# Kernel tuning notes

Measured on AMD Instinct MI355X. Metric: run time of the kernel, lower is better.

## Reference

```python
import jax, jax.numpy as jnp
import numpy as np

D_MODEL = 768
N_HEAD = 12
D_FF = 2048
KEEP_RATIO = 0.6
EPS = 1e-6


def rmsnorm(x, g):
    var = jnp.mean(x * x, axis=-1, keepdims=True)
    return x * jax.lax.rsqrt(var + EPS) * g


def setup_inputs() -> dict:
    key = jax.random.key(0)
    ks = jax.random.split(key, 16)
    B, S, D, F = 2, 2048, D_MODEL, D_FF
    s = 0.02
    inp = {
        "hidden": jax.random.normal(ks[0], (B, S, D), jnp.float32),
        "attn_mask": jnp.tril(jnp.ones((S, S), dtype=bool)),
        "temperature": 1,
        "wq": jax.random.normal(ks[1], (D, D), jnp.float32) * s,
        "wk": jax.random.normal(ks[2], (D, D), jnp.float32) * s,
        "wv": jax.random.normal(ks[3], (D, D), jnp.float32) * s,
        "wo": jax.random.normal(ks[4], (D, D), jnp.float32) * s,
        "w1": jax.random.normal(ks[5], (D, F), jnp.float32) * s,
        "w3": jax.random.normal(ks[6], (D, F), jnp.float32) * s,
        "w2": jax.random.normal(ks[7], (F, D), jnp.float32) * s,
        "g1": jnp.ones((D,), jnp.float32),
        "g2": jnp.ones((D,), jnp.float32),
        "w_mod": jax.random.normal(ks[8], (D,), jnp.float32) * s,
        "b_mod": jnp.zeros((), jnp.float32),
        "w_tok": jax.random.normal(ks[9], (D,), jnp.float32) * s,
        "b_tok": jnp.zeros((), jnp.float32),
        "w_gate": jax.random.normal(ks[10], (D, D), jnp.float32) * s,
        "b_gate": jnp.zeros((D,), jnp.float32),
    }
    return inp


def reference(hidden, attn_mask, temperature, wq, wk, wv, wo, w1, w3, w2,
              g1, g2, w_mod, b_mod, w_tok, b_tok, w_gate, b_gate):
    B, S, D = hidden.shape
    H = N_HEAD
    Dh = D // H

    # depth router: sigmoid(linear / temperature)
    depth_logits = jnp.einsum("bsd,d->bs", hidden, w_mod) + b_mod
    depth_probs = jax.nn.sigmoid(depth_logits / temperature)
    active = (depth_probs > 0.5).astype(hidden.dtype)[..., None]  # [B,S,1]

    normed = rmsnorm(hidden, g1)

    # token router: sigmoid scores, hard top-k keep mask at base keep ratio
    token_scores = jax.nn.sigmoid(jnp.einsum("bsd,d->bs", normed, w_tok) + b_tok)
    k = max(1, int(S * KEEP_RATIO))
    kth = jax.lax.top_k(token_scores, k)[0][:, -1:]  # [B,1]
    token_mask = (token_scores >= kth).astype(hidden.dtype)  # [B,S]

    # multi-head attention over normed
    q = jnp.einsum("bsd,de->bse", normed, wq).reshape(B, S, H, Dh)
    kk = jnp.einsum("bsd,de->bse", normed, wk).reshape(B, S, H, Dh)
    v = jnp.einsum("bsd,de->bse", normed, wv).reshape(B, S, H, Dh)
    logits = jnp.einsum("bqhd,bkhd->bhqk", q, kk) / jnp.sqrt(jnp.float32(Dh))
    logits = jnp.where(attn_mask[None, None, :, :], logits, jnp.float32(-1e9))
    probs = jax.nn.softmax(logits, axis=-1)
    ctx = jnp.einsum("bhqk,bkhd->bqhd", probs, v).reshape(B, S, D)
    attn_out = jnp.einsum("bsd,de->bse", ctx, wo)

    attn_out = attn_out * token_mask[..., None]
    hidden = hidden + attn_out * active  # dropout = identity (eval)

    # ACM gate: x * sigmoid(Wx + b)
    n2 = rmsnorm(hidden, g2)
    gated = n2 * jax.nn.sigmoid(jnp.einsum("bsd,de->bse", n2, w_gate) + b_gate)

    # SwiGLU MLP
    mlp = jnp.einsum("bsf,fd->bsd",
                     jax.nn.silu(jnp.einsum("bsd,df->bsf", gated, w1))
                     * jnp.einsum("bsd,df->bsf", gated, w3), w2)
    hidden = hidden + mlp * active
    return hidden, depth_probs, token_mask
```

## Files before the change

kernel.cpp:

```cpp
#include <hip/hip_runtime.h>


typedef float f32x4 __attribute__((ext_vector_type(4)));
typedef __bf16 bf16x8 __attribute__((ext_vector_type(8)));
typedef __bf16 bf16x4 __attribute__((ext_vector_type(4)));
typedef unsigned int u32;

#define DEV static __device__ __forceinline__

constexpr int SEQ = 2048, DIM = 768, NH = 12;
constexpr int KKEEP = 1228;
constexpr float SCALE2 = 0.125f * 1.4426950408889634f;

DEV f32x4 mfma16(bf16x8 a, bf16x8 b, f32x4 c) {
  return __builtin_amdgcn_mfma_f32_16x16x32_bf16(a, b, c, 0, 0, 0);
}
DEV float sigm(float x) { return 1.0f / (1.0f + __expf(-x)); }
DEV bf16x8 ld8(const __bf16* p) { return *reinterpret_cast<const bf16x8*>(p); }
DEV void st8(__bf16* p, bf16x8 v) { *reinterpret_cast<bf16x8*>(p) = v; }
DEV int swzo(int row, int u) { return row * 64 + ((u ^ (row & 7)) << 3); }

template <int NZ>
struct PtrPack { const float* s[NZ]; };

template <int NZ>
__global__ void k_transpose_castz(PtrPack<NZ> pp, __bf16* __restrict__ dst0,
                                  int K, int N, size_t dstride) {
  const float* __restrict__ src = pp.s[blockIdx.z];
  __bf16* __restrict__ dst = dst0 + (size_t)blockIdx.z * dstride;
  __shared__ float tile[32][33];
  const int tx = threadIdx.x, ty = threadIdx.y;
  const int n0 = blockIdx.x * 32, k0 = blockIdx.y * 32;
  for (int i = 0; i < 4; ++i)
    tile[ty + 8 * i][tx] = src[(size_t)(k0 + ty + 8 * i) * N + n0 + tx];
  __syncthreads();
  for (int i = 0; i < 4; ++i)
    dst[(size_t)(n0 + ty + 8 * i) * K + k0 + tx] = (__bf16)tile[tx][ty + 8 * i];
}

__global__ __launch_bounds__(256) void k_router(
    const float* __restrict__ hid, const float* __restrict__ g1,
    const float* __restrict__ wmod, const float* __restrict__ bmod,
    const float* __restrict__ wtok, const float* __restrict__ btok,
    const int* __restrict__ temp, __bf16* __restrict__ normed,
    float* __restrict__ depth_out, float* __restrict__ actF,
    float* __restrict__ tokL) {
  const int t = blockIdx.x, tid = threadIdx.x;
  const float* x = hid + (size_t)t * DIM;
  float xs[3], gs[3], ss = 0.f, dm = 0.f, dt = 0.f;
  for (int j = 0; j < 3; ++j) {
    const int i = tid + 256 * j;
    const float xv = x[i], g = g1[i];
    xs[j] = xv; gs[j] = g;
    ss += xv * xv;
    dm += xv * wmod[i];
    dt += xv * g * wtok[i];
  }
  for (int m = 32; m >= 1; m >>= 1) {
    ss += __shfl_xor(ss, m);
    dm += __shfl_xor(dm, m);
    dt += __shfl_xor(dt, m);
  }
  __shared__ float red[4][3];
  if ((tid & 63) == 0) { red[tid >> 6][0] = ss; red[tid >> 6][1] = dm; red[tid >> 6][2] = dt; }
  __syncthreads();
  ss = red[0][0] + red[1][0] + red[2][0] + red[3][0];
  dm = red[0][1] + red[1][1] + red[2][1] + red[3][1];
  dt = red[0][2] + red[1][2] + red[2][2] + red[3][2];
  const float rms = rsqrtf(ss / 768.0f + 1e-6f);
  if (tid == 0) {
    const int iv = temp[0];
    const float T = (iv > -100000 && iv < 100000) ? (float)iv : __int_as_float(iv);
    const float z = (dm + bmod[0]) / T;
    depth_out[t] = sigm(z);
    actF[t] = z > 0.0f ? 1.0f : 0.0f;
    tokL[t] = rms * dt + btok[0];
  }
  for (int j = 0; j < 3; ++j) {
    const int i = tid + 256 * j;
    normed[(size_t)t * DIM + i] = (__bf16)(xs[j] * rms * gs[j]);
  }
}

__global__ __launch_bounds__(256) void k_count(
    const float* __restrict__ tokL, float* __restrict__ kth_out) {
  const int b = blockIdx.y, tid = threadIdx.x;
  __shared__ float vals[2048];
  const float* L = tokL + (size_t)b * 2048;
#pragma unroll
  for (int j = 0; j < 8; ++j) vals[tid + 256 * j] = L[tid + 256 * j];
  __syncthreads();
  const int cand = blockIdx.x * 128 + (tid >> 1);
  const int half = tid & 1;
  const float e = vals[cand];
  int gt = 0, ge = 0;
  const float4* v4 = reinterpret_cast<const float4*>(vals) + half * 256;
#pragma unroll 8
  for (int j = 0; j < 256; ++j) {
    const float4 q = v4[j];
    gt += (q.x > e) + (q.y > e) + (q.z > e) + (q.w > e);
    ge += (q.x >= e) + (q.y >= e) + (q.z >= e) + (q.w >= e);
  }
  gt += __shfl_xor(gt, 1);
  ge += __shfl_xor(ge, 1);
  if (half == 0 && gt < KKEEP && KKEEP <= ge) kth_out[b] = e;
}

__global__ __launch_bounds__(256) void k_mask(
    const float* __restrict__ tokL, const float* __restrict__ kth,
    const float* __restrict__ actF, float* __restrict__ mask_out,
    float* __restrict__ maskact) {
  const int i = blockIdx.x * 256 + threadIdx.x;
  const int b = i >> 11;
  const float m = (tokL[i] >= kth[b]) ? 1.f : 0.f;
  mask_out[i] = m;
  maskact[i] = m * actF[i];
}

__global__ __launch_bounds__(256) void k_rmsnorm2(
    const float* __restrict__ h2, const float* __restrict__ g2,
    __bf16* __restrict__ n2) {
  const int t = blockIdx.x, tid = threadIdx.x;
  const float* x = h2 + (size_t)t * DIM;
  float xs[3], ss = 0.f;
  for (int j = 0; j < 3; ++j) { const float v = x[tid + 256 * j]; xs[j] = v; ss += v * v; }
  for (int m = 32; m >= 1; m >>= 1) ss += __shfl_xor(ss, m);
  __shared__ float red[4];
  if ((tid & 63) == 0) red[tid >> 6] = ss;
  __syncthreads();
  ss = red[0] + red[1] + red[2] + red[3];
  const float rms = rsqrtf(ss / 768.0f + 1e-6f);
  for (int j = 0; j < 3; ++j) {
    const int i = tid + 256 * j;
    n2[(size_t)t * DIM + i] = (__bf16)(xs[j] * rms * g2[i]);
  }
}

template <int EPI, int MI, int NI>
__global__ __launch_bounds__(256) void k_gemm(
    const __bf16* __restrict__ A, const __bf16* __restrict__ BT,
    int N, int K, size_t bt_stride, size_t out_stride,
    __bf16* __restrict__ outB, float* __restrict__ outF,
    const float* __restrict__ epF, const __bf16* __restrict__ epB,
    const float* __restrict__ rowsc, const float* __restrict__ bias) {
  constexpr int BM = MI * 32, BN = NI * 32;
  __shared__ __align__(16) __bf16 As[BM * 64];
  __shared__ __align__(16) __bf16 Bs[BN * 64];
  const int tid = threadIdx.x;
  const int lane = tid & 63, w = tid >> 6;
  const int wr = w >> 1, wc = w & 1;
  const int f = lane & 15, e = lane >> 4;
  const int m0 = blockIdx.y * BM, n0 = blockIdx.x * BN;
  const __bf16* Bz = BT + (size_t)blockIdx.z * bt_stride;

  const int rowA = (MI == 4) ? (tid >> 1) : (tid >> 2);
  const int uA0  = (MI == 4) ? ((tid & 1) * 4) : ((tid & 3) * 2);
  const int rowB = (NI == 4) ? (tid >> 1) : (tid >> 2);
  const int uB0  = (NI == 4) ? ((tid & 1) * 4) : ((tid & 3) * 2);
  const __bf16* ApR = A + (size_t)(m0 + rowA) * K;
  const __bf16* BpR = Bz + (size_t)(n0 + rowB) * K;

  bf16x8 ya[MI], yb[NI];
  auto LOADY = [&](int k0) {
#pragma unroll
    for (int j = 0; j < MI; ++j) ya[j] = ld8(ApR + k0 + (uA0 + j) * 8);
#pragma unroll
    for (int j = 0; j < NI; ++j) yb[j] = ld8(BpR + k0 + (uB0 + j) * 8);
  };
  auto STORE = [&]() {
#pragma unroll
    for (int j = 0; j < MI; ++j) st8(&As[swzo(rowA, uA0 + j)], ya[j]);
#pragma unroll
    for (int j = 0; j < NI; ++j) st8(&Bs[swzo(rowB, uB0 + j)], yb[j]);
  };

  f32x4 acc[MI][NI] = {};
  LOADY(0);
  for (int k0 = 0; k0 < K; k0 += 64) {
    __syncthreads();
    STORE();
    if (k0 + 64 < K) LOADY(k0 + 64);
    __syncthreads();
    bf16x8 afl[MI], afh[MI], bfl[NI], bfh[NI];
#pragma unroll
    for (int mi = 0; mi < MI; ++mi) {
      const int row = wr * (MI * 16) + mi * 16 + f;
      afl[mi] = ld8(&As[swzo(row, e)]);
      afh[mi] = ld8(&As[swzo(row, e + 4)]);
    }
#pragma unroll
    for (int ni = 0; ni < NI; ++ni) {
      const int row = wc * (NI * 16) + ni * 16 + f;
      bfl[ni] = ld8(&Bs[swzo(row, e)]);
      bfh[ni] = ld8(&Bs[swzo(row, e + 4)]);
    }
#pragma unroll
    for (int mi = 0; mi < MI; ++mi)
#pragma unroll
      for (int ni = 0; ni < NI; ++ni) {
        acc[mi][ni] = mfma16(afl[mi], bfl[ni], acc[mi][ni]);
        acc[mi][ni] = mfma16(afh[mi], bfh[ni], acc[mi][ni]);
      }
  }
  const size_t oz = (size_t)blockIdx.z * out_stride;
  if constexpr (EPI == 5) {
    __bf16* vt = (__bf16*)outF;
    const bool isv = (blockIdx.z == 2);
    const float qs = (blockIdx.z == 0) ? SCALE2 : 1.0f;
#pragma unroll
    for (int mi = 0; mi < MI; ++mi)
#pragma unroll
      for (int ni = 0; ni < NI; ++ni) {
        const int row0 = m0 + wr * (MI * 16) + mi * 16 + e * 4;
        const int col = n0 + wc * (NI * 16) + ni * 16 + f;
        if (!isv) {
#pragma unroll
          for (int r2 = 0; r2 < 4; ++r2)
            outB[oz + (size_t)(row0 + r2) * N + col] =
                (__bf16)(acc[mi][ni][r2] * qs);
        } else {
          bf16x4 pk;
#pragma unroll
          for (int r2 = 0; r2 < 4; ++r2) pk[r2] = (__bf16)acc[mi][ni][r2];
          *reinterpret_cast<bf16x4*>(&vt[(size_t)col * 4096 + row0]) = pk;
        }
      }
  } else {
#pragma unroll
    for (int mi = 0; mi < MI; ++mi)
#pragma unroll
      for (int ni = 0; ni < NI; ++ni)
#pragma unroll
        for (int r2 = 0; r2 < 4; ++r2) {
          const int row = m0 + wr * (MI * 16) + mi * 16 + e * 4 + r2;
          const int col = n0 + wc * (NI * 16) + ni * 16 + f;
          const size_t idx = (size_t)row * N + col;
          const float c = acc[mi][ni][r2];
          if constexpr (EPI == 0) {
            outB[oz + idx] = (__bf16)c;
          } else if constexpr (EPI == 1) {
            outF[idx] = epF[idx] + c * rowsc[row];
          } else if constexpr (EPI == 2) {
            outB[idx] = (__bf16)((float)epB[idx] * sigm(c + bias[col]));
          }
        }
  }
}

__global__ __launch_bounds__(256) void k_gemm13(
    const __bf16* __restrict__ A, const __bf16* __restrict__ B1T,
    const __bf16* __restrict__ B3T, __bf16* __restrict__ outT) {
  __shared__ __align__(16) __bf16 As[64 * 64];
  __shared__ __align__(16) __bf16 B1s[128 * 64];
  __shared__ __align__(16) __bf16 B3s[128 * 64];
  const int tid = threadIdx.x;
  const int lane = tid & 63, w = tid >> 6;
  const int wr = w >> 1, wc = w & 1;
  const int f = lane & 15, e = lane >> 4;
  const int m0 = blockIdx.y * 64, n0 = blockIdx.x * 128;
  const int rowA = tid >> 2, uA0 = (tid & 3) * 2;
  const int rowB = tid >> 1, uB0 = (tid & 1) * 4;
  const __bf16* ApR = A + (size_t)(m0 + rowA) * 768;
  const __bf16* B1R = B1T + (size_t)(n0 + rowB) * 768;
  const __bf16* B3R = B3T + (size_t)(n0 + rowB) * 768;

  bf16x8 ya[2], yb1[4], yb3[4];
  auto LOADY = [&](int k0) {
#pragma unroll
    for (int j = 0; j < 2; ++j) ya[j] = ld8(ApR + k0 + (uA0 + j) * 8);
#pragma unroll
    for (int j = 0; j < 4; ++j) yb1[j] = ld8(B1R + k0 + (uB0 + j) * 8);
#pragma unroll
    for (int j = 0; j < 4; ++j) yb3[j] = ld8(B3R + k0 + (uB0 + j) * 8);
  };
  auto STORE = [&]() {
#pragma unroll
    for (int j = 0; j < 2; ++j) st8(&As[swzo(rowA, uA0 + j)], ya[j]);
#pragma unroll
    for (int j = 0; j < 4; ++j) st8(&B1s[swzo(rowB, uB0 + j)], yb1[j]);
#pragma unroll
    for (int j = 0; j < 4; ++j) st8(&B3s[swzo(rowB, uB0 + j)], yb3[j]);
  };

  f32x4 acc1[2][4] = {}, acc3[2][4] = {};
  LOADY(0);
  for (int k0 = 0; k0 < 768; k0 += 64) {
    __syncthreads();
    STORE();
    if (k0 + 64 < 768) LOADY(k0 + 64);
    __syncthreads();
    bf16x8 afl[2], afh[2], bl[4], bh[4];
#pragma unroll
    for (int mi = 0; mi < 2; ++mi) {
      const int row = wr * 32 + mi * 16 + f;
      afl[mi] = ld8(&As[swzo(row, e)]);
      afh[mi] = ld8(&As[swzo(row, e + 4)]);
    }
#pragma unroll
    for (int ni = 0; ni < 4; ++ni) {
      const int row = wc * 64 + ni * 16 + f;
      bl[ni] = ld8(&B1s[swzo(row, e)]);
      bh[ni] = ld8(&B1s[swzo(row, e + 4)]);
    }
#pragma unroll
    for (int mi = 0; mi < 2; ++mi)
#pragma unroll
      for (int ni = 0; ni < 4; ++ni) {
        acc1[mi][ni] = mfma16(afl[mi], bl[ni], acc1[mi][ni]);
        acc1[mi][ni] = mfma16(afh[mi], bh[ni], acc1[mi][ni]);
      }
#pragma unroll
    for (int ni = 0; ni < 4; ++ni) {
      const int row = wc * 64 + ni * 16 + f;
      bl[ni] = ld8(&B3s[swzo(row, e)]);
      bh[ni] = ld8(&B3s[swzo(row, e + 4)]);
    }
#pragma unroll
    for (int mi = 0; mi < 2; ++mi)
#pragma unroll
      for (int ni = 0; ni < 4; ++ni) {
        acc3[mi][ni] = mfma16(afl[mi], bl[ni], acc3[mi][ni]);
        acc3[mi][ni] = mfma16(afh[mi], bh[ni], acc3[mi][ni]);
      }
  }
#pragma unroll
  for (int mi = 0; mi < 2; ++mi)
#pragma unroll
    for (int ni = 0; ni < 4; ++ni)
#pragma unroll
      for (int r2 = 0; r2 < 4; ++r2) {
        const int row = m0 + wr * 32 + mi * 16 + e * 4 + r2;
        const int col = n0 + wc * 64 + ni * 16 + f;
        const float u = acc1[mi][ni][r2];
        outT[(size_t)row * 2048 + col] = (__bf16)(u * sigm(u) * acc3[mi][ni][r2]);
      }
}

__global__ __launch_bounds__(256) void k_attn(
    const __bf16* __restrict__ qb, const __bf16* __restrict__ kb,
    const __bf16* __restrict__ vT, __bf16* __restrict__ Opart,
    float* __restrict__ ml) {
  __shared__ __bf16 Ks[64 * 64];
  __shared__ __bf16 Vt[64 * 64];
  __shared__ __bf16 Pl[4][16][72];
  const int tid = threadIdx.x, lane = tid & 63, w = tid >> 6;
  const int f = lane & 15, e = lane >> 4;
  const int idx = 79 - (int)blockIdx.x;
  int g4, rel;
  if (idx < 8)       { g4 = 0; rel = idx; }
  else if (idx < 24) { g4 = 1; rel = idx - 8; }
  else if (idx < 48) { g4 = 2; rel = idx - 24; }
  else               { g4 = 3; rel = idx - 48; }
  const int qt = (g4 << 3) + rel / (g4 + 1);
  const int c  = rel % (g4 + 1);
  const int bh = blockIdx.y;
  const int b = bh / NH, h = bh % NH;
  const int slot = bh * 80 + idx;
  const int q0 = qt * 64;
  const int kt0 = c * 8;
  const int ntile = min(8, qt + 1 - kt0);
  const size_t base = (size_t)b * SEQ * DIM + (size_t)h * 64;

  const int qrow = q0 + w * 16 + f;
  const bf16x8 aq0 = ld8(qb + base + (size_t)qrow * DIM + e * 8);
  const bf16x8 aq1 = ld8(qb + base + (size_t)qrow * DIM + 32 + e * 8);
  float lsum[4] = {0.f, 0.f, 0.f, 0.f};
  f32x4 cacc[4];
  for (int g = 0; g < 4; ++g) cacc[g] = f32x4{0.f, 0.f, 0.f, 0.f};

  const int r1 = tid >> 2, u0 = tid & 3;
  const __bf16* kp = kb + base + (size_t)r1 * DIM;
  const __bf16* vp = vT + (size_t)(h * 64 + r1) * 4096 + b * 2048;

  bf16x8 rk0 = ld8(kp + (size_t)(kt0 * 64) * DIM + u0 * 8);
  bf16x8 rk1 = ld8(kp + (size_t)(kt0 * 64) * DIM + (u0 + 4) * 8);
  bf16x8 rv0 = ld8(vp + kt0 * 64 + u0 * 8);
  bf16x8 rv1 = ld8(vp + kt0 * 64 + (u0 + 4) * 8);

  for (int tt = 0; tt < ntile; ++tt) {
    const int kt = kt0 + tt;
    __syncthreads();
    st8(&Ks[swzo(r1, u0)], rk0);  st8(&Ks[swzo(r1, u0 + 4)], rk1);
    st8(&Vt[swzo(r1, u0)], rv0);  st8(&Vt[swzo(r1, u0 + 4)], rv1);
    if (tt + 1 < ntile) {
      const size_t ko = (size_t)((kt + 1) * 64) * DIM;
      rk0 = ld8(kp + ko + u0 * 8);  rk1 = ld8(kp + ko + (u0 + 4) * 8);
      const int vo = (kt + 1) * 64;
      rv0 = ld8(vp + vo + u0 * 8);  rv1 = ld8(vp + vo + (u0 + 4) * 8);
    }
    __syncthreads();

    f32x4 sacc[4];
#pragma unroll
    for (int g = 0; g < 4; ++g) {
      const int row = g * 16 + f;
      f32x4 z = f32x4{0.f, 0.f, 0.f, 0.f};
      z = mfma16(aq0, ld8(&Ks[swzo(row, e)]), z);
      z = mfma16(aq1, ld8(&Ks[swzo(row, e + 4)]), z);
      sacc[g] = z;
    }
    const bool need_mask = (kt == qt);
    const int qg = q0 + w * 16 + e * 4;
    float p[4][4];
#pragma unroll
    for (int g = 0; g < 4; ++g) {
      const int kg = kt * 64 + g * 16 + f;
#pragma unroll
      for (int r = 0; r < 4; ++r) {
        const float pv = (need_mask && (kg > qg + r))
                             ? 0.f
                             : exp2f(sacc[g][r]);
        p[g][r] = pv;
        lsum[r] += pv;
      }
    }
#pragma unroll
    for (int g = 0; g < 4; ++g)
#pragma unroll
      for (int r = 0; r < 4; ++r) Pl[w][e * 4 + r][g * 16 + f] = (__bf16)p[g][r];
    const bf16x8 ap0 = ld8(&Pl[w][f][e * 8]);
    const bf16x8 ap1 = ld8(&Pl[w][f][32 + e * 8]);
#pragma unroll
    for (int g = 0; g < 4; ++g) {
      const int row = g * 16 + f;
      cacc[g] = mfma16(ap0, ld8(&Vt[swzo(row, e)]), cacc[g]);
      cacc[g] = mfma16(ap1, ld8(&Vt[swzo(row, e + 4)]), cacc[g]);
    }
  }
  for (int m = 1; m < 16; m <<= 1)
#pragma unroll
    for (int r = 0; r < 4; ++r) lsum[r] += __shfl_xor(lsum[r], m);
  if (f == 0) {
#pragma unroll
    for (int r = 0; r < 4; ++r)
      ml[(size_t)slot * 64 + w * 16 + e * 4 + r] = lsum[r];
  }
#pragma unroll
  for (int g = 0; g < 4; ++g)
#pragma unroll
    for (int r = 0; r < 4; ++r) {
      const int row = w * 16 + e * 4 + r;
      Opart[(size_t)slot * 4096 + row * 64 + g * 16 + f] = (__bf16)cacc[g][r];
    }
}

__global__ __launch_bounds__(256) void k_attn_combine(
    const __bf16* __restrict__ Opart, const float* __restrict__ ml,
    __bf16* __restrict__ ctxb) {
  const int qt = blockIdx.x, bh = blockIdx.y;
  const int b = bh / NH, h = bh % NH;
  const int g = qt >> 3;
  const int sb = bh * 80 + 4 * g * (g + 1) + (qt & 7) * (g + 1);
  const int nch = g + 1;
  const int row = threadIdx.x >> 2, dh0 = (threadIdx.x & 3) * 16;

  float ltot = 0.f;
  float acc[16];
#pragma unroll
  for (int j = 0; j < 16; ++j) acc[j] = 0.f;
  for (int cc = 0; cc < nch; ++cc) {
    ltot += ml[(size_t)(sb + cc) * 64 + row];
    const __bf16* op = Opart + (size_t)(sb + cc) * 4096 + row * 64 + dh0;
    const bf16x8 o0 = ld8(op), o1 = ld8(op + 8);
#pragma unroll
    for (int j = 0; j < 8; ++j) {
      acc[j] += (float)o0[j];
      acc[8 + j] += (float)o1[j];
    }
  }
  const float rl = 1.0f / ltot;
  bf16x8 w0, w1;
#pragma unroll
  for (int j = 0; j < 8; ++j) {
    w0[j] = (__bf16)(acc[j] * rl);
    w1[j] = (__bf16)(acc[8 + j] * rl);
  }
  const size_t base = (size_t)b * SEQ * DIM + (size_t)h * 64;
  __bf16* dst = ctxb + base + (size_t)(qt * 64 + row) * DIM + dh0;
  st8(dst, w0);
  st8(dst + 8, w1);
}

extern "C" void kernel_launch(void* const* d_in, const int* in_sizes, int n_in,
                              void* d_out, int out_size, void* d_ws, size_t ws_size,
                              hipStream_t stream) {
  const float* hid   = (const float*)d_in[0];
  const int*   temp  = (const int*)d_in[2];
  const float* wq    = (const float*)d_in[3];
  const float* wk    = (const float*)d_in[4];
  const float* wv    = (const float*)d_in[5];
  const float* wo    = (const float*)d_in[6];
  const float* w1    = (const float*)d_in[7];
  const float* w3    = (const float*)d_in[8];
  const float* w2    = (const float*)d_in[9];
  const float* g1    = (const float*)d_in[10];
  const float* g2    = (const float*)d_in[11];
  const float* wmod  = (const float*)d_in[12];
  const float* bmod  = (const float*)d_in[13];
  const float* wtok  = (const float*)d_in[14];
  const float* btok  = (const float*)d_in[15];
  const float* wgate = (const float*)d_in[16];
  const float* bgate = (const float*)d_in[17];

  char* ws = (char*)d_ws;
  __bf16* WT = (__bf16*)ws;
  const size_t oWQ = 0, oWK = 589824, oWV = 1179648, oWO = 1769472,
               oWG = 2359296, oW1 = 2949120, oW3 = 4521984, oW2 = 6094848;
  __bf16* qbuf   = (__bf16*)(ws + 15335424);
  __bf16* kbuf   = qbuf + 3145728;
  __bf16* vTbuf  = kbuf + 3145728;
  __bf16* normed = (__bf16*)(ws + 34209792);
  __bf16* ctxb   = normed + 3145728;
  __bf16* n2buf  = ctxb + 3145728;
  __bf16* tbuf   = normed;
  float*  h2     = (float*)(ws + 53084160);
  __bf16* gated  = (__bf16*)(ws + 65667072);
  __bf16* Opart  = (__bf16*)(ws + 53084160);
  float*  mlbuf  = (float*)(ws + 68812800);
  float*  tokL   = (float*)(ws + 71958528);
  float*  actF   = tokL + 4096;
  float*  maskact = actF + 4096;
  float*  kthbuf  = maskact + 4096;

  float* dout = (float*)d_out;
  float* out_hidden = dout;
  float* out_depth  = dout + 3145728;
  float* out_mask   = dout + 3145728 + 4096;

  const dim3 tb(32, 8);
  PtrPack<5> p5; p5.s[0]=wq; p5.s[1]=wk; p5.s[2]=wv; p5.s[3]=wo; p5.s[4]=wgate;
  k_transpose_castz<5><<<dim3(24, 24, 5), tb, 0, stream>>>(p5, WT + oWQ, 768, 768, 589824);
  PtrPack<2> p2; p2.s[0]=w1; p2.s[1]=w3;
  k_transpose_castz<2><<<dim3(64, 24, 2), tb, 0, stream>>>(p2, WT + oW1, 768, 2048, 1572864);
  PtrPack<1> p1; p1.s[0]=w2;
  k_transpose_castz<1><<<dim3(24, 64, 1), tb, 0, stream>>>(p1, WT + oW2, 2048, 768, 0);

  k_router<<<4096, 256, 0, stream>>>(hid, g1, wmod, bmod, wtok, btok, temp,
                                     normed, out_depth, actF, tokL);
  k_count<<<dim3(16, 2), 256, 0, stream>>>(tokL, kthbuf);
  k_mask<<<16, 256, 0, stream>>>(tokL, kthbuf, actF, out_mask, maskact);

  k_gemm<5, 4, 4><<<dim3(6, 32, 3), 256, 0, stream>>>(
      normed, WT + oWQ, 768, 768, 589824, 3145728,
      qbuf, (float*)vTbuf, nullptr, nullptr, nullptr, nullptr);

  k_attn<<<dim3(80, 24), 256, 0, stream>>>(qbuf, kbuf, vTbuf, Opart, mlbuf);
  k_attn_combine<<<dim3(32, 24), 256, 0, stream>>>(Opart, mlbuf, ctxb);

  k_gemm<1, 2, 2><<<dim3(12, 64, 1), 256, 0, stream>>>(
      ctxb, WT + oWO, 768, 768, 0, 0,
      nullptr, h2, hid, nullptr, maskact, nullptr);

  k_rmsnorm2<<<4096, 256, 0, stream>>>(h2, g2, n2buf);

  k_gemm<2, 2, 2><<<dim3(12, 64, 1), 256, 0, stream>>>(
      n2buf, WT + oWG, 768, 768, 0, 0,
      gated, nullptr, nullptr, n2buf, nullptr, bgate);

  k_gemm13<<<dim3(16, 64), 256, 0, stream>>>(gated, WT + oW1, WT + oW3, tbuf);

  k_gemm<1, 2, 2><<<dim3(12, 64, 1), 256, 0, stream>>>(
      tbuf, WT + oW2, 768, 2048, 0, 0,
      nullptr, out_hidden, h2, nullptr, actF, nullptr);

  (void)in_sizes; (void)n_in; (void)out_size; (void)ws_size;
}
```

Before: 199.9 us.

## Interleave W1/W3 columns and reuse generic GEMM with a SwiGLU epilogue

The w1 and w3 weights are transposed into one row-interleaved matrix, so a single generic GEMM with N=4096 computes both projections. A new epilogue pairs adjacent columns with a lane shuffle and writes silu(u)*v. This replaces the dedicated dual-B gemm13 kernel with the larger-tile 4x4 GEMM path. Separately, the attention loop splits the diagonal-masked tile from unmasked tiles so the mask compare is skipped off the diagonal. In exchange, half the lanes sit idle during the SwiGLU store.

```diff
diff --git a/kernel.cpp b/kernel.cpp
--- a/kernel.cpp
+++ b/kernel.cpp
@@ -23,19 +23,25 @@
 template <int NZ>
 struct PtrPack { const float* s[NZ]; };
 
-template <int NZ>
+template <int NZ, int ILV = 0>
 __global__ void k_transpose_castz(PtrPack<NZ> pp, __bf16* __restrict__ dst0,
                                   int K, int N, size_t dstride) {
   const float* __restrict__ src = pp.s[blockIdx.z];
-  __bf16* __restrict__ dst = dst0 + (size_t)blockIdx.z * dstride;
   __shared__ float tile[32][33];
   const int tx = threadIdx.x, ty = threadIdx.y;
   const int n0 = blockIdx.x * 32, k0 = blockIdx.y * 32;
   for (int i = 0; i < 4; ++i)
     tile[ty + 8 * i][tx] = src[(size_t)(k0 + ty + 8 * i) * N + n0 + tx];
   __syncthreads();
-  for (int i = 0; i < 4; ++i)
-    dst[(size_t)(n0 + ty + 8 * i) * K + k0 + tx] = (__bf16)tile[tx][ty + 8 * i];
+  if constexpr (ILV) {
+    for (int i = 0; i < 4; ++i)
+      dst0[((size_t)(n0 + ty + 8 * i) * 2 + blockIdx.z) * K + k0 + tx] =
+          (__bf16)tile[tx][ty + 8 * i];
+  } else {
+    __bf16* __restrict__ dst = dst0 + (size_t)blockIdx.z * dstride;
+    for (int i = 0; i < 4; ++i)
+      dst[(size_t)(n0 + ty + 8 * i) * K + k0 + tx] = (__bf16)tile[tx][ty + 8 * i];
+  }
 }
 
 __global__ __launch_bounds__(256) void k_router(
@@ -225,6 +231,22 @@
           *reinterpret_cast<bf16x4*>(&vt[(size_t)col * 4096 + row0]) = pk;
         }
       }
+  } else if constexpr (EPI == 6) {
+    const int NO = N >> 1;
+#pragma unroll
+    for (int mi = 0; mi < MI; ++mi)
+#pragma unroll
+      for (int ni = 0; ni < NI; ++ni)
+#pragma unroll
+        for (int r2 = 0; r2 < 4; ++r2) {
+          const float mine = acc[mi][ni][r2];
+          const float part = __shfl_xor(mine, 1);
+          if ((f & 1) == 0) {
+            const int row = m0 + wr * (MI * 16) + mi * 16 + e * 4 + r2;
+            const int j = (n0 + wc * (NI * 16) + ni * 16 + f) >> 1;
+            outB[(size_t)row * NO + j] = (__bf16)(mine * sigm(mine) * part);
+          }
+        }
   } else {
 #pragma unroll
     for (int mi = 0; mi < MI; ++mi)
@@ -245,95 +267,6 @@
           }
         }
   }
-}
-
-__global__ __launch_bounds__(256) void k_gemm13(
-    const __bf16* __restrict__ A, const __bf16* __restrict__ B1T,
-    const __bf16* __restrict__ B3T, __bf16* __restrict__ outT) {
-  __shared__ __align__(16) __bf16 As[64 * 64];
-  __shared__ __align__(16) __bf16 B1s[128 * 64];
-  __shared__ __align__(16) __bf16 B3s[128 * 64];
-  const int tid = threadIdx.x;
-  const int lane = tid & 63, w = tid >> 6;
-  const int wr = w >> 1, wc = w & 1;
-  const int f = lane & 15, e = lane >> 4;
-  const int m0 = blockIdx.y * 64, n0 = blockIdx.x * 128;
-  const int rowA = tid >> 2, uA0 = (tid & 3) * 2;
-  const int rowB = tid >> 1, uB0 = (tid & 1) * 4;
-  const __bf16* ApR = A + (size_t)(m0 + rowA) * 768;
-  const __bf16* B1R = B1T + (size_t)(n0 + rowB) * 768;
-  const __bf16* B3R = B3T + (size_t)(n0 + rowB) * 768;
-
-  bf16x8 ya[2], yb1[4], yb3[4];
-  auto LOADY = [&](int k0) {
-#pragma unroll
-    for (int j = 0; j < 2; ++j) ya[j] = ld8(ApR + k0 + (uA0 + j) * 8);
-#pragma unroll
-    for (int j = 0; j < 4; ++j) yb1[j] = ld8(B1R + k0 + (uB0 + j) * 8);
-#pragma unroll
-    for (int j = 0; j < 4; ++j) yb3[j] = ld8(B3R + k0 + (uB0 + j) * 8);
-  };
-  auto STORE = [&]() {
-#pragma unroll
-    for (int j = 0; j < 2; ++j) st8(&As[swzo(rowA, uA0 + j)], ya[j]);
-#pragma unroll
-    for (int j = 0; j < 4; ++j) st8(&B1s[swzo(rowB, uB0 + j)], yb1[j]);
-#pragma unroll
-    for (int j = 0; j < 4; ++j) st8(&B3s[swzo(rowB, uB0 + j)], yb3[j]);
-  };
-
-  f32x4 acc1[2][4] = {}, acc3[2][4] = {};
-  LOADY(0);
-  for (int k0 = 0; k0 < 768; k0 += 64) {
-    __syncthreads();
-    STORE();
-    if (k0 + 64 < 768) LOADY(k0 + 64);
-    __syncthreads();
-    bf16x8 afl[2], afh[2], bl[4], bh[4];
-#pragma unroll
-    for (int mi = 0; mi < 2; ++mi) {
-      const int row = wr * 32 + mi * 16 + f;
-      afl[mi] = ld8(&As[swzo(row, e)]);
-      afh[mi] = ld8(&As[swzo(row, e + 4)]);
-    }
-#pragma unroll
-    for (int ni = 0; ni < 4; ++ni) {
-      const int row = wc * 64 + ni * 16 + f;
-      bl[ni] = ld8(&B1s[swzo(row, e)]);
-      bh[ni] = ld8(&B1s[swzo(row, e + 4)]);
-    }
-#pragma unroll
-    for (int mi = 0; mi < 2; ++mi)
-#pragma unroll
-      for (int ni = 0; ni < 4; ++ni) {
-        acc1[mi][ni] = mfma16(afl[mi], bl[ni], acc1[mi][ni]);
-        acc1[mi][ni] = mfma16(afh[mi], bh[ni], acc1[mi][ni]);
-      }
-#pragma unroll
-    for (int ni = 0; ni < 4; ++ni) {
-      const int row = wc * 64 + ni * 16 + f;
-      bl[ni] = ld8(&B3s[swzo(row, e)]);
-      bh[ni] = ld8(&B3s[swzo(row, e + 4)]);
-    }
-#pragma unroll
-    for (int mi = 0; mi < 2; ++mi)
-#pragma unroll
-      for (int ni = 0; ni < 4; ++ni) {
-        acc3[mi][ni] = mfma16(afl[mi], bl[ni], acc3[mi][ni]);
-        acc3[mi][ni] = mfma16(afh[mi], bh[ni], acc3[mi][ni]);
-      }
-  }
-#pragma unroll
-  for (int mi = 0; mi < 2; ++mi)
-#pragma unroll
-    for (int ni = 0; ni < 4; ++ni)
-#pragma unroll
-      for (int r2 = 0; r2 < 4; ++r2) {
-        const int row = m0 + wr * 32 + mi * 16 + e * 4 + r2;
-        const int col = n0 + wc * 64 + ni * 16 + f;
-        const float u = acc1[mi][ni][r2];
-        outT[(size_t)row * 2048 + col] = (__bf16)(u * sigm(u) * acc3[mi][ni][r2]);
-      }
 }
 
 __global__ __launch_bounds__(256) void k_attn(
@@ -399,20 +332,28 @@
       z = mfma16(aq1, ld8(&Ks[swzo(row, e + 4)]), z);
       sacc[g] = z;
     }
-    const bool need_mask = (kt == qt);
-    const int qg = q0 + w * 16 + e * 4;
     float p[4][4];
-#pragma unroll
-    for (int g = 0; g < 4; ++g) {
-      const int kg = kt * 64 + g * 16 + f;
-#pragma unroll
-      for (int r = 0; r < 4; ++r) {
-        const float pv = (need_mask && (kg > qg + r))
-                             ? 0.f
-                             : exp2f(sacc[g][r]);
-        p[g][r] = pv;
-        lsum[r] += pv;
+    if (kt == qt) {
+      const int qg = q0 + w * 16 + e * 4;
+#pragma unroll
+      for (int g = 0; g < 4; ++g) {
+        const int kg = kt * 64 + g * 16 + f;
+#pragma unroll
+        for (int r = 0; r < 4; ++r) {
+          const float pv = (kg > qg + r) ? 0.f : exp2f(sacc[g][r]);
+          p[g][r] = pv;
+          lsum[r] += pv;
+        }
       }
+    } else {
+#pragma unroll
+      for (int g = 0; g < 4; ++g)
+#pragma unroll
+        for (int r = 0; r < 4; ++r) {
+          const float pv = exp2f(sacc[g][r]);
+          p[g][r] = pv;
+          lsum[r] += pv;
+        }
     }
 #pragma unroll
     for (int g = 0; g < 4; ++g)
@@ -505,7 +446,7 @@
   char* ws = (char*)d_ws;
   __bf16* WT = (__bf16*)ws;
   const size_t oWQ = 0, oWK = 589824, oWV = 1179648, oWO = 1769472,
-               oWG = 2359296, oW1 = 2949120, oW3 = 4521984, oW2 = 6094848;
+               oWG = 2359296, oW13 = 2949120, oW2 = 6094848;
   __bf16* qbuf   = (__bf16*)(ws + 15335424);
   __bf16* kbuf   = qbuf + 3145728;
   __bf16* vTbuf  = kbuf + 3145728;
@@ -531,7 +472,7 @@
   PtrPack<5> p5; p5.s[0]=wq; p5.s[1]=wk; p5.s[2]=wv; p5.s[3]=wo; p5.s[4]=wgate;
   k_transpose_castz<5><<<dim3(24, 24, 5), tb, 0, stream>>>(p5, WT + oWQ, 768, 768, 589824);
   PtrPack<2> p2; p2.s[0]=w1; p2.s[1]=w3;
-  k_transpose_castz<2><<<dim3(64, 24, 2), tb, 0, stream>>>(p2, WT + oW1, 768, 2048, 1572864);
+  k_transpose_castz<2, 1><<<dim3(64, 24, 2), tb, 0, stream>>>(p2, WT + oW13, 768, 2048, 0);
   PtrPack<1> p1; p1.s[0]=w2;
   k_transpose_castz<1><<<dim3(24, 64, 1), tb, 0, stream>>>(p1, WT + oW2, 2048, 768, 0);
 
@@ -557,7 +498,9 @@
       n2buf, WT + oWG, 768, 768, 0, 0,
       gated, nullptr, nullptr, n2buf, nullptr, bgate);
 
-  k_gemm13<<<dim3(16, 64), 256, 0, stream>>>(gated, WT + oW1, WT + oW3, tbuf);
+  k_gemm<6, 4, 4><<<dim3(32, 32, 1), 256, 0, stream>>>(
+      gated, WT + oW13, 4096, 768, 0, 0,
+      tbuf, nullptr, nullptr, nullptr, nullptr, nullptr);
 
   k_gemm<1, 2, 2><<<dim3(12, 64, 1), 256, 0, stream>>>(
       tbuf, WT + oW2, 768, 2048, 0, 0,
```

New measurement: 197.7 us. No clear change (-1.1%).
